# Kernel tuning notes

Measured on AMD Instinct MI355X. Metric: run time of the kernel, lower is better.

Reference implementation:

```python
import jax, jax.numpy as jnp
import numpy as np

N = 1024  # num boxes (labels == predictions count so diff == 0 branch)


def jaccard(box_a, box_b):
    # box_a: [A,4], box_b: [B,4], xyxy format -> IoU matrix [A,B]
    max_xy = jnp.minimum(box_a[:, None, 2:], box_b[None, :, 2:])
    min_xy = jnp.maximum(box_a[:, None, :2], box_b[None, :, :2])
    inter_wh = jnp.clip(max_xy - min_xy, 0.0)
    inter = inter_wh[..., 0] * inter_wh[..., 1]
    area_a = ((box_a[:, 2] - box_a[:, 0]) * (box_a[:, 3] - box_a[:, 1]))[:, None]
    area_b = ((box_b[:, 2] - box_b[:, 0]) * (box_b[:, 3] - box_b[:, 1]))[None, :]
    return inter / (area_a + area_b - inter)


def greedy_match(JM):
    """Replicates the original greedy loop: N steps; each step takes the LAST
    row-major-order maximal entry ('>=' update) among rows/cols not in `seen`,
    swaps label rows r<->c (tracked via perm), and marks column c as seen."""
    n = JM.shape[0]
    MASKED = jnp.float32(-1.0)  # IoU >= 0, so -1 excludes masked entries

    def body(carry, _):
        perm, seen = carry
        M = JM[perm]                                  # rows permuted with labels
        mask = seen[:, None] | seen[None, :]          # one `seen` set for rows & cols
        vals = jnp.where(mask, MASKED, M).reshape(-1)
        # last occurrence of the max (the '>=' in the Python loop keeps the latest)
        i = vals.shape[0] - 1 - jnp.argmax(vals[::-1])
        r, c = i // n, i % n
        pr, pc = perm[r], perm[c]
        perm = perm.at[r].set(pc).at[c].set(pr)
        seen = seen.at[c].set(True)
        return (perm, seen), None

    init = (jnp.arange(n), jnp.zeros(n, dtype=bool))
    (perm, _), _ = jax.lax.scan(body, init, None, length=n)
    return perm


def setup_inputs() -> dict:
    key = jax.random.key(0)
    k1, k2, k3, k4, k5 = jax.random.split(key, 5)
    # valid xyxy boxes: x2 > x1, y2 > y1
    lmin = jax.random.uniform(k1, (N, 2), dtype=jnp.float32)
    lwh = jax.random.uniform(k2, (N, 2), dtype=jnp.float32) * 0.2 + 0.01
    labels = jnp.concatenate([lmin, lmin + lwh], axis=-1)
    pmin = jax.random.uniform(k3, (N, 2), dtype=jnp.float32)
    pwh = jax.random.uniform(k4, (N, 2), dtype=jnp.float32) * 0.2 + 0.01
    predictions = jnp.concatenate([pmin, pmin + pwh], axis=-1)
    scores = jax.random.normal(k5, (N,), dtype=jnp.float32)
    return {"predictions": predictions, "labels": labels, "scores": scores}


def reference(predictions, labels, scores):
    # L == P -> diff == 0, no truncation, scores untouched.
    JM = jaccard(labels, predictions)
    perm = greedy_match(JM)
    labels_matched = labels[perm]
    # F.l1_loss default reduction: mean over all elements.
    # NOTE: the original's `loss.add(F.cross_entropy(...))` is non-in-place and
    # its result is discarded, so the CE term does NOT contribute; diff == 0 so
    # the diff*4 branch is skipped. Faithfully: loss = L1 only.
    loss = jnp.mean(jnp.abs(labels_matched - predictions))
    return loss
```

## Files before the change

kernel.cpp:

```cpp
#include <hip/hip_runtime.h>
#include <stdint.h>

#define NBOX 1024

typedef unsigned long long u64;
typedef unsigned int u32;
typedef unsigned short u16;
typedef unsigned char u8;

__device__ __forceinline__ float iou_pair(const float4 lb, float larea,
                                          const float4 pb, float parea) {
    float ix1 = fmaxf(lb.x, pb.x);
    float iy1 = fmaxf(lb.y, pb.y);
    float ix2 = fminf(lb.z, pb.z);
    float iy2 = fminf(lb.w, pb.w);
    float w = fmaxf(__fsub_rn(ix2, ix1), 0.0f);
    float h = fmaxf(__fsub_rn(iy2, iy1), 0.0f);
    float inter = __fmul_rn(w, h);
    float denom = __fsub_rn(__fadd_rn(larea, parea), inter);
    return inter / denom;
}

__device__ __forceinline__ u64 umax64(u64 a, u64 b) { return a > b ? a : b; }

__device__ __forceinline__ u64 dpp_max64(u64 v) {
    unsigned lo, hi; u64 o;
#define DPP_STEP(CTRL) \
    lo = (unsigned)__builtin_amdgcn_update_dpp(0, (int)(unsigned)(v & 0xffffffffull), CTRL, 0xf, 0xf, true); \
    hi = (unsigned)__builtin_amdgcn_update_dpp(0, (int)(unsigned)(v >> 32),           CTRL, 0xf, 0xf, true); \
    o = (((u64)hi) << 32) | lo; \
    if (o > v) v = o;
    DPP_STEP(0x111) DPP_STEP(0x112) DPP_STEP(0x114)
    DPP_STEP(0x118) DPP_STEP(0x142) DPP_STEP(0x143)
#undef DPP_STEP
    return v;
}

__device__ __forceinline__ u64 readlane64(u64 v, int l) {
    unsigned lo = (unsigned)__builtin_amdgcn_readlane((int)(unsigned)(v & 0xffffffffull), l);
    unsigned hi = (unsigned)__builtin_amdgcn_readlane((int)(unsigned)(v >> 32), l);
    return (((u64)hi) << 32) | lo;
}

__global__ void __launch_bounds__(64) init_rowlist(const float* __restrict__ labels,
                                                   const float* __restrict__ preds,
                                                   u64* __restrict__ rowlist) {
    const int b = blockIdx.x;
    const int lane = threadIdx.x;
    float4 lb = ((const float4*)labels)[b];
    float la = __fmul_rn(__fsub_rn(lb.z, lb.x), __fsub_rn(lb.w, lb.y));
    u32 vb[16];
    #pragma unroll
    for (int j = 0; j < 16; ++j) {
        int c = lane + (j << 6);
        float4 pb = ((const float4*)preds)[c];
        float pa = __fmul_rn(__fsub_rn(pb.z, pb.x), __fsub_rn(pb.w, pb.y));
        vb[j] = __float_as_uint(iou_pair(lb, la, pb, pa));
    }
    u32 used = 0;
    for (int it = 0; it < 8; ++it) {
        u64 best = 0;
        #pragma unroll
        for (int j = 0; j < 16; ++j) {
            if (!((used >> j) & 1u)) {
                u64 p = ((u64)vb[j] << 10) | (u32)(lane + (j << 6));
                best = umax64(best, p);
            }
        }
        best = dpp_max64(best);
        u64 bm = readlane64(best, 63);
        if ((bm >> 10) == 0ull) bm = 0;
        if (lane == 0) rowlist[(b << 3) + it] = bm;
        if (bm && (int)(bm & 63) == lane) used |= 1u << ((bm >> 6) & 15);
    }
}

__global__ void __launch_bounds__(64) init_collist(const float* __restrict__ labels,
                                                   const float* __restrict__ preds,
                                                   u64* __restrict__ collist) {
    const int c = blockIdx.x;
    const int lane = threadIdx.x;
    float4 pc = ((const float4*)preds)[c];
    float pa = __fmul_rn(__fsub_rn(pc.z, pc.x), __fsub_rn(pc.w, pc.y));
    u32 vb[16];
    #pragma unroll
    for (int j = 0; j < 16; ++j) {
        int L = lane + (j << 6);
        float4 lb = ((const float4*)labels)[L];
        float la = __fmul_rn(__fsub_rn(lb.z, lb.x), __fsub_rn(lb.w, lb.y));
        vb[j] = __float_as_uint(iou_pair(lb, la, pc, pa));
    }
    u32 used = 0;
    for (int it = 0; it < 8; ++it) {
        u64 best = 0;
        #pragma unroll
        for (int j = 0; j < 16; ++j) {
            if (!((used >> j) & 1u)) {
                u64 p = ((u64)vb[j] << 10) | (u32)(lane + (j << 6));
                best = umax64(best, p);
            }
        }
        best = dpp_max64(best);
        u64 bm = readlane64(best, 63);
        if ((bm >> 10) == 0ull) bm = 0;
        if (lane == 0) collist[(c << 3) + it] = bm;
        if (bm && (int)(bm & 63) == lane) used |= 1u << ((bm >> 6) & 15);
    }
}

__global__ void __launch_bounds__(1024, 1)
rounds_kernel(const float* __restrict__ preds,
              const float* __restrict__ labels,
              const u64* __restrict__ rowlist,
              const u64* __restrict__ collist,
              float* __restrict__ out) {
    __shared__ float4 pred4s[NBOX];
    __shared__ float4 lab4s[NBOX];
    __shared__ float  parea_s[NBOX];
    __shared__ float  larea_s[NBOX];
    __shared__ u64    rkey[NBOX];
    __shared__ u64    colbest[NBOX];
    __shared__ u16    dest_s[NBOX];
    __shared__ u16    perm_s[NBOX];
    __shared__ u8     seenc[NBOX];
    __shared__ u8     lockedl[NBOX];
    __shared__ u32    seenw[32];
    __shared__ u32    lockedw[32];
    __shared__ int    ncom[2];
    __shared__ float  fpart[16];

    const int t    = (int)threadIdx.x;
    const int lane = t & 63;
    const int wid  = t >> 6;

    {
        float4 p = ((const float4*)preds)[t];
        float4 L = ((const float4*)labels)[t];
        pred4s[t] = p;
        lab4s[t]  = L;
        parea_s[t] = __fmul_rn(__fsub_rn(p.z, p.x), __fsub_rn(p.w, p.y));
        larea_s[t] = __fmul_rn(__fsub_rn(L.z, L.x), __fsub_rn(L.w, L.y));
        perm_s[t] = (u16)t; dest_s[t] = 0;
        seenc[t] = 0; lockedl[t] = 0;
        rkey[t] = rowlist ? rowlist[t << 3] : 0ull;
        colbest[t] = 0ull;
        if (t < 32) { seenw[t] = 0u; lockedw[t] = 0u; }
        if (t < 2) ncom[t] = 0;
    }
    __syncthreads();

    u32 myseen = 0;
    u32 mylocked = 0;
    int rptr = rowlist ? 0 : 8;
    int cptr = collist ? 0 : 8;
    int par = 0;

    auto rebuild_seen = [&]() {
        u32 ms = 0;
        #pragma unroll
        for (int m = 0; m < 4; ++m) {
            u32 w_ = seenw[(lane >> 3) + (m << 3)];
            ms |= ((w_ >> ((lane & 7) << 2)) & 0xFu) << (m << 2);
        }
        myseen = ms;
    };
    auto rebuild_locked = [&]() {
        u32 ml = 0;
        #pragma unroll
        for (int m = 0; m < 4; ++m) {
            u32 w_ = lockedw[(lane >> 3) + (m << 3)];
            ml |= ((w_ >> ((lane & 7) << 2)) & 0xFu) << (m << 2);
        }
        mylocked = ml;
    };

    auto scan_row_exact = [&](int row) -> u64 {
        float4 lbx = lab4s[row];
        float la = larea_s[row];
        u64 best = 0;
        #pragma unroll
        for (int m = 0; m < 4; ++m) {
            #pragma unroll
            for (int k = 0; k < 4; ++k) {
                int cc = 4 * lane + 256 * m + k;
                float v = iou_pair(lbx, la, pred4s[cc], parea_s[cc]);
                u64 p = ((u64)__float_as_uint(v) << 10) | (unsigned)cc;
                if ((myseen >> ((m << 2) | k)) & 1u) p = 0;
                best = umax64(best, p);
            }
        }
        best = dpp_max64(best);
        u64 bm = readlane64(best, 63);
        return (bm >> 10) ? bm : 0ull;
    };

    auto scan_col_exact = [&](int c) -> u64 {
        float4 pc = pred4s[c];
        float  pa = parea_s[c];
        u64 best = 0; u32 v1 = 0, v2 = 0;
        #pragma unroll
        for (int m = 0; m < 4; ++m) {
            #pragma unroll
            for (int k = 0; k < 4; ++k) {
                int L = 4 * lane + 256 * m + k;
                float v = iou_pair(lab4s[L], larea_s[L], pc, pa);
                u32 vbb = __float_as_uint(v);
                if ((mylocked >> ((m << 2) | k)) & 1u) vbb = 0;
                if (vbb >= v1) { v2 = v1; v1 = vbb; } else { v2 = (vbb > v2) ? vbb : v2; }
                best = umax64(best, ((u64)vbb << 10) | (unsigned)L);
            }
        }
        best = dpp_max64(best);
        u64 bm = readlane64(best, 63);
        u32 V = (u32)(bm >> 10);
        if (!V) return 0ull;
        u64 b1 = __ballot(v1 == V);
        u64 b2 = __ballot(v2 == V);
        bool tie = (__popcll(b1) >= 2) || (b2 != 0ull);
        return ((u64)V << 32) | (tie ? (1ull << 16) : 0ull) | (bm & 1023ull);
    };

    auto do_commit = [&](int c, int L) {
        seenc[c] = 1; lockedl[L] = 1; rkey[L] = 0ull;
        dest_s[L] = (u16)c; perm_s[c] = (u16)L;
        atomicOr(&seenw[c >> 5], 1u << (c & 31));
        atomicOr(&lockedw[L >> 5], 1u << (L & 31));
        atomicAdd(&ncom[par], 1);
    };

    if (!rowlist) {
        for (int row = wid; row < NBOX; row += 16) {
            u64 r = scan_row_exact(row);
            if (lane == 0) rkey[row] = r;
        }
        __syncthreads();
    }

    {
        u64 k = rkey[t];
        if (k) atomicMax((unsigned long long*)&colbest[k & 1023ull],
                         ((k >> 10) << 10) | (u64)(unsigned)t);
    }
    __syncthreads();

    for (int round = 0; round < 4096; ++round) {
        par = round & 1;

        u64 sb = colbest[t];
        {
            colbest[t] = 0ull;
            bool needexact = false;
            if (sb) {
                if (cptr >= 8) {
                    needexact = true;
                } else {
                    u32 V = 0, lab1 = 0; bool dead = false;
                    int i = cptr;
                    for (; i < 8; ++i) {
                        u64 e = collist[(t << 3) + i];
                        u32 v = (u32)(e >> 10);
                        if (!v) { dead = true; break; }
                        u32 lb = (u32)(e & 1023ull);
                        if (!lockedl[lb]) { V = v; lab1 = lb; break; }
                    }
                    cptr = i;
                    if (!dead) {
                        if (i >= 8) {
                            needexact = true;
                        } else {
                            bool tie = false;
                            int j = i + 1;
                            for (; j < 8; ++j) {
                                u64 e2 = collist[(t << 3) + j];
                                u32 v2 = (u32)(e2 >> 10);
                                if (v2 != V) break;
                                if (!lockedl[e2 & 1023ull]) { tie = true; break; }
                            }
                            if (!tie && j >= 8) needexact = true;
                            if (!needexact && !tie) {
                                if ((u32)(sb & 1023ull) == lab1) do_commit(t, (int)lab1);
                            }
                        }
                    }
                }
            }
            u64 bal = __ballot(needexact);
            if (bal) {
                rebuild_locked();
                while (bal) {
                    int l = (int)__ffsll(bal) - 1; bal &= bal - 1;
                    int c = (wid << 6) | l;
                    u64 o = scan_col_exact(c);
                    u64 sbl = readlane64(sb, l);
                    if (lane == 0) {
                        u32 Vx = (u32)(o >> 32);
                        if (Vx && !((o >> 16) & 1ull) &&
                            (u32)(o & 1023ull) == (u32)(sbl & 1023ull))
                            do_commit(c, (int)(o & 1023ull));
                    }
                }
            }
        }
        __syncthreads();

        const int cnt = ncom[par];
        if (t == 0) ncom[par ^ 1] = 0;
        if (cnt == 0) break;
        {
            bool needscan = false;
            u64 k = rkey[t];
            if (k && seenc[k & 1023ull]) {
                if (rptr >= 8) {
                    needscan = true;
                } else {
                    int i = rptr; u64 nk = 0;
                    for (; i < 8; ++i) {
                        u64 e = rowlist[(t << 3) + i];
                        if ((e >> 10) == 0ull) break;
                        if (!seenc[e & 1023ull]) { nk = e; break; }
                    }
                    if (i < 8) { rkey[t] = nk; rptr = i; }
                    else { rptr = 8; needscan = true; }
                }
            }
            u64 bal = __ballot(needscan);
            if (bal) {
                rebuild_seen();
                while (bal) {
                    int l = (int)__ffsll(bal) - 1; bal &= bal - 1;
                    int row = (wid << 6) | l;
                    u64 r = scan_row_exact(row);
                    if (lane == 0) rkey[row] = r;
                }
            }
            u64 k2 = rkey[t];
            if (k2) atomicMax((unsigned long long*)&colbest[k2 & 1023ull],
                              ((k2 >> 10) << 10) | (u64)(unsigned)t);
        }
        __syncthreads();
    }

    if (!seenc[t]) {
        int l = t;
        while (lockedl[l]) l = (int)dest_s[l];
        perm_s[t] = (u16)l;
    }
    __syncthreads();

    {
        float4 lb = lab4s[perm_s[t]];
        float4 pb = pred4s[t];
        float sum = fabsf(lb.x - pb.x) + fabsf(lb.y - pb.y) +
                    fabsf(lb.z - pb.z) + fabsf(lb.w - pb.w);
        for (int off = 32; off > 0; off >>= 1) sum += __shfl_xor(sum, off, 64);
        if (lane == 0) fpart[wid] = sum;
        __syncthreads();
        if (t == 0) {
            float s = 0.0f;
            for (int w = 0; w < 16; ++w) s += fpart[w];
            out[0] = s * (1.0f / 4096.0f);
        }
    }
}

extern "C" void kernel_launch(void* const* d_in, const int* in_sizes, int n_in,
                              void* d_out, int out_size, void* d_ws, size_t ws_size,
                              hipStream_t stream) {
    const float* preds  = (const float*)d_in[0];
    const float* labels = (const float*)d_in[1];
    float* out = (float*)d_out;

    const size_t list_b = (size_t)NBOX * 8 * sizeof(u64);
    if (d_ws && ws_size >= 2 * list_b) {
        u64* rl = (u64*)d_ws;
        u64* cl = rl + NBOX * 8;
        init_rowlist<<<NBOX, 64, 0, stream>>>(labels, preds, rl);
        init_collist<<<NBOX, 64, 0, stream>>>(labels, preds, cl);
        rounds_kernel<<<1, 1024, 0, stream>>>(preds, labels, rl, cl, out);
    } else {
        rounds_kernel<<<1, 1024, 0, stream>>>(preds, labels, nullptr, nullptr, out);
    }
}
```

Before: 221.8 us.

## Halve rounds-kernel block to 512 threads, two columns per thread, cache collist in registers

The single-block greedy-matching kernel now runs with 512 threads, each handling two boxes/columns, which cuts the cost of each __syncthreads barrier across the many rounds. Each thread's 8-entry column candidate lists are preloaded into registers once. The per-round column walk becomes a branch-light unrolled check over all 8 entries instead of a pointer-advancing loop over global memory. The risks are higher register pressure, serialization of per-thread work across two items, and possible semantic drift in the tie/exhaustion logic versus the old cursor-based walk.

```diff
diff --git a/kernel.cpp b/kernel.cpp
--- a/kernel.cpp
+++ b/kernel.cpp
@@ -2,6 +2,7 @@
 #include <stdint.h>
 
 #define NBOX 1024
+#define BLK  512
 
 typedef unsigned long long u64;
 typedef unsigned int u32;
@@ -108,7 +109,7 @@
     }
 }
 
-__global__ void __launch_bounds__(1024, 1)
+__global__ void __launch_bounds__(BLK, 1)
 rounds_kernel(const float* __restrict__ preds,
               const float* __restrict__ labels,
               const u64* __restrict__ rowlist,
@@ -127,33 +128,50 @@
     __shared__ u32    seenw[32];
     __shared__ u32    lockedw[32];
     __shared__ int    ncom[2];
-    __shared__ float  fpart[16];
+    __shared__ float  fpart[8];
 
     const int t    = (int)threadIdx.x;
     const int lane = t & 63;
     const int wid  = t >> 6;
 
-    {
-        float4 p = ((const float4*)preds)[t];
-        float4 L = ((const float4*)labels)[t];
-        pred4s[t] = p;
-        lab4s[t]  = L;
-        parea_s[t] = __fmul_rn(__fsub_rn(p.z, p.x), __fsub_rn(p.w, p.y));
-        larea_s[t] = __fmul_rn(__fsub_rn(L.z, L.x), __fsub_rn(L.w, L.y));
-        perm_s[t] = (u16)t; dest_s[t] = 0;
-        seenc[t] = 0; lockedl[t] = 0;
-        rkey[t] = rowlist ? rowlist[t << 3] : 0ull;
-        colbest[t] = 0ull;
-        if (t < 32) { seenw[t] = 0u; lockedw[t] = 0u; }
-        if (t < 2) ncom[t] = 0;
-    }
+    #pragma unroll
+    for (int s = 0; s < 2; ++s) {
+        int i = t + (s << 9);
+        float4 p = ((const float4*)preds)[i];
+        float4 L = ((const float4*)labels)[i];
+        pred4s[i] = p;
+        lab4s[i]  = L;
+        parea_s[i] = __fmul_rn(__fsub_rn(p.z, p.x), __fsub_rn(p.w, p.y));
+        larea_s[i] = __fmul_rn(__fsub_rn(L.z, L.x), __fsub_rn(L.w, L.y));
+        perm_s[i] = (u16)i; dest_s[i] = 0;
+        seenc[i] = 0; lockedl[i] = 0;
+        rkey[i] = rowlist ? rowlist[i << 3] : 0ull;
+        colbest[i] = 0ull;
+    }
+    if (t < 32) { seenw[t] = 0u; lockedw[t] = 0u; }
+    if (t < 2) ncom[t] = 0;
     __syncthreads();
+
+    u32 cvA[8], clA[8], cvB[8], clB[8];
+    if (collist) {
+        #pragma unroll
+        for (int k = 0; k < 8; ++k) {
+            u64 e = collist[(t << 3) + k];
+            cvA[k] = (u32)(e >> 10); clA[k] = (u32)(e & 1023ull);
+            e = collist[((t + 512) << 3) + k];
+            cvB[k] = (u32)(e >> 10); clB[k] = (u32)(e & 1023ull);
+        }
+    } else {
+        #pragma unroll
+        for (int k = 0; k < 8; ++k) { cvA[k] = clA[k] = cvB[k] = clB[k] = 0; }
+    }
 
     u32 myseen = 0;
     u32 mylocked = 0;
-    int rptr = rowlist ? 0 : 8;
-    int cptr = collist ? 0 : 8;
+    int rptr0 = rowlist ? 0 : 8;
+    int rptr1 = rowlist ? 0 : 8;
     int par = 0;
+    const bool havelists = (collist != nullptr);
 
     auto rebuild_seen = [&]() {
         u32 ms = 0;
@@ -228,78 +246,86 @@
         atomicAdd(&ncom[par], 1);
     };
 
+#define COLWALK(CV, CL, cidx, sbv, needx) do { \
+        if (!havelists) { needx = true; } else { \
+            bool lk_[8]; \
+            _Pragma("unroll") \
+            for (int k = 0; k < 8; ++k) lk_[k] = lockedl[CL[k]]; \
+            u32 fm_ = 0; \
+            _Pragma("unroll") \
+            for (int k = 0; k < 8; ++k) if (CV[k] && !lk_[k]) fm_ |= 1u << k; \
+            if (!fm_) { if (CV[7]) needx = true;  } \
+            else { \
+                u32 V_ = 0, lab_ = 0; \
+                _Pragma("unroll") \
+                for (int k = 7; k >= 0; --k) \
+                    if ((fm_ >> k) & 1u) { V_ = CV[k]; lab_ = CL[k]; } \
+                u32 eq_ = 0; \
+                _Pragma("unroll") \
+                for (int k = 0; k < 8; ++k) if (CV[k] == V_) eq_ |= 1u << k; \
+                bool tie_ = __popc(fm_ & eq_) >= 2; \
+                if (!tie_) { \
+                    if (CV[7] == V_) needx = true;               \
+                    else if ((u32)((sbv) & 1023ull) == lab_) do_commit((cidx), (int)lab_); \
+                }  \
+            } \
+        } } while (0)
+
     if (!rowlist) {
-        for (int row = wid; row < NBOX; row += 16) {
+        for (int row = wid; row < NBOX; row += 8) {
             u64 r = scan_row_exact(row);
             if (lane == 0) rkey[row] = r;
         }
         __syncthreads();
     }
 
-    {
-        u64 k = rkey[t];
+    #pragma unroll
+    for (int s = 0; s < 2; ++s) {
+        u64 k = rkey[t + (s << 9)];
         if (k) atomicMax((unsigned long long*)&colbest[k & 1023ull],
-                         ((k >> 10) << 10) | (u64)(unsigned)t);
+                         ((k >> 10) << 10) | (u64)(unsigned)(t + (s << 9)));
     }
     __syncthreads();
 
     for (int round = 0; round < 4096; ++round) {
         par = round & 1;
 
-        u64 sb = colbest[t];
         {
-            colbest[t] = 0ull;
-            bool needexact = false;
-            if (sb) {
-                if (cptr >= 8) {
-                    needexact = true;
-                } else {
-                    u32 V = 0, lab1 = 0; bool dead = false;
-                    int i = cptr;
-                    for (; i < 8; ++i) {
-                        u64 e = collist[(t << 3) + i];
-                        u32 v = (u32)(e >> 10);
-                        if (!v) { dead = true; break; }
-                        u32 lb = (u32)(e & 1023ull);
-                        if (!lockedl[lb]) { V = v; lab1 = lb; break; }
-                    }
-                    cptr = i;
-                    if (!dead) {
-                        if (i >= 8) {
-                            needexact = true;
-                        } else {
-                            bool tie = false;
-                            int j = i + 1;
-                            for (; j < 8; ++j) {
-                                u64 e2 = collist[(t << 3) + j];
-                                u32 v2 = (u32)(e2 >> 10);
-                                if (v2 != V) break;
-                                if (!lockedl[e2 & 1023ull]) { tie = true; break; }
-                            }
-                            if (!tie && j >= 8) needexact = true;
-                            if (!needexact && !tie) {
-                                if ((u32)(sb & 1023ull) == lab1) do_commit(t, (int)lab1);
-                            }
-                        }
-                    }
-                }
-            }
-            u64 bal = __ballot(needexact);
+            u64 sb0 = colbest[t];       colbest[t] = 0ull;
+            u64 sb1 = colbest[t + 512]; colbest[t + 512] = 0ull;
+            bool ne0 = false, ne1 = false;
+            if (sb0) COLWALK(cvA, clA, t, sb0, ne0);
+            if (sb1) COLWALK(cvB, clB, t + 512, sb1, ne1);
+            u64 bal = __ballot(ne0);
             if (bal) {
                 rebuild_locked();
                 while (bal) {
                     int l = (int)__ffsll(bal) - 1; bal &= bal - 1;
                     int c = (wid << 6) | l;
                     u64 o = scan_col_exact(c);
-                    u64 sbl = readlane64(sb, l);
+                    u64 sbl = readlane64(sb0, l);
                     if (lane == 0) {
-                        u32 Vx = (u32)(o >> 32);
-                        if (Vx && !((o >> 16) & 1ull) &&
+                        if ((o >> 32) && !((o >> 16) & 1ull) &&
                             (u32)(o & 1023ull) == (u32)(sbl & 1023ull))
                             do_commit(c, (int)(o & 1023ull));
                     }
                 }
             }
+            bal = __ballot(ne1);
+            if (bal) {
+                rebuild_locked();
+                while (bal) {
+                    int l = (int)__ffsll(bal) - 1; bal &= bal - 1;
+                    int c = 512 + ((wid << 6) | l);
+                    u64 o = scan_col_exact(c);
+                    u64 sbl = readlane64(sb1, l);
+                    if (lane == 0) {
+                        if ((o >> 32) && !((o >> 16) & 1ull) &&
+                            (u32)(o & 1023ull) == (u32)(sbl & 1023ull))
+                            do_commit(c, (int)(o & 1023ull));
+                    }
+                }
+            }
         }
         __syncthreads();
 
@@ -307,23 +333,30 @@
         if (t == 0) ncom[par ^ 1] = 0;
         if (cnt == 0) break;
         {
-            bool needscan = false;
-            u64 k = rkey[t];
-            if (k && seenc[k & 1023ull]) {
-                if (rptr >= 8) {
-                    needscan = true;
-                } else {
-                    int i = rptr; u64 nk = 0;
-                    for (; i < 8; ++i) {
-                        u64 e = rowlist[(t << 3) + i];
-                        if ((e >> 10) == 0ull) break;
-                        if (!seenc[e & 1023ull]) { nk = e; break; }
+            bool ns0 = false, ns1 = false;
+            #pragma unroll
+            for (int s = 0; s < 2; ++s) {
+                int row = t + (s << 9);
+                int rp = s ? rptr1 : rptr0;
+                bool needscan = false;
+                u64 k = rkey[row];
+                if (k && seenc[k & 1023ull]) {
+                    if (rp >= 8) {
+                        needscan = true;
+                    } else {
+                        int i = rp; u64 nk = 0;
+                        for (; i < 8; ++i) {
+                            u64 e = rowlist[(row << 3) + i];
+                            if ((e >> 10) == 0ull) break;
+                            if (!seenc[e & 1023ull]) { nk = e; break; }
+                        }
+                        if (i < 8) { rkey[row] = nk; rp = i; }
+                        else { rp = 8; needscan = true; }
                     }
-                    if (i < 8) { rkey[t] = nk; rptr = i; }
-                    else { rptr = 8; needscan = true; }
                 }
-            }
-            u64 bal = __ballot(needscan);
+                if (s) { rptr1 = rp; ns1 = needscan; } else { rptr0 = rp; ns0 = needscan; }
+            }
+            u64 bal = __ballot(ns0);
             if (bal) {
                 rebuild_seen();
                 while (bal) {
@@ -333,31 +366,54 @@
                     if (lane == 0) rkey[row] = r;
                 }
             }
-            u64 k2 = rkey[t];
-            if (k2) atomicMax((unsigned long long*)&colbest[k2 & 1023ull],
-                              ((k2 >> 10) << 10) | (u64)(unsigned)t);
+            bal = __ballot(ns1);
+            if (bal) {
+                rebuild_seen();
+                while (bal) {
+                    int l = (int)__ffsll(bal) - 1; bal &= bal - 1;
+                    int row = 512 + ((wid << 6) | l);
+                    u64 r = scan_row_exact(row);
+                    if (lane == 0) rkey[row] = r;
+                }
+            }
+            #pragma unroll
+            for (int s = 0; s < 2; ++s) {
+                int row = t + (s << 9);
+                u64 k2 = rkey[row];
+                if (k2) atomicMax((unsigned long long*)&colbest[k2 & 1023ull],
+                                  ((k2 >> 10) << 10) | (u64)(unsigned)row);
+            }
         }
         __syncthreads();
     }
 
-    if (!seenc[t]) {
-        int l = t;
-        while (lockedl[l]) l = (int)dest_s[l];
-        perm_s[t] = (u16)l;
+    #pragma unroll
+    for (int s = 0; s < 2; ++s) {
+        int i = t + (s << 9);
+        if (!seenc[i]) {
+            int l = i;
+            while (lockedl[l]) l = (int)dest_s[l];
+            perm_s[i] = (u16)l;
+        }
     }
     __syncthreads();
 
     {
-        float4 lb = lab4s[perm_s[t]];
-        float4 pb = pred4s[t];
-        float sum = fabsf(lb.x - pb.x) + fabsf(lb.y - pb.y) +
-                    fabsf(lb.z - pb.z) + fabsf(lb.w - pb.w);
+        float sum = 0.0f;
+        #pragma unroll
+        for (int s = 0; s < 2; ++s) {
+            int i = t + (s << 9);
+            float4 lb = lab4s[perm_s[i]];
+            float4 pb = pred4s[i];
+            sum += fabsf(lb.x - pb.x) + fabsf(lb.y - pb.y) +
+                   fabsf(lb.z - pb.z) + fabsf(lb.w - pb.w);
+        }
         for (int off = 32; off > 0; off >>= 1) sum += __shfl_xor(sum, off, 64);
         if (lane == 0) fpart[wid] = sum;
         __syncthreads();
         if (t == 0) {
             float s = 0.0f;
-            for (int w = 0; w < 16; ++w) s += fpart[w];
+            for (int w = 0; w < 8; ++w) s += fpart[w];
             out[0] = s * (1.0f / 4096.0f);
         }
     }
@@ -376,8 +432,8 @@
         u64* cl = rl + NBOX * 8;
         init_rowlist<<<NBOX, 64, 0, stream>>>(labels, preds, rl);
         init_collist<<<NBOX, 64, 0, stream>>>(labels, preds, cl);
-        rounds_kernel<<<1, 1024, 0, stream>>>(preds, labels, rl, cl, out);
+        rounds_kernel<<<1, BLK, 0, stream>>>(preds, labels, rl, cl, out);
     } else {
-        rounds_kernel<<<1, 1024, 0, stream>>>(preds, labels, nullptr, nullptr, out);
-    }
-}
+        rounds_kernel<<<1, BLK, 0, stream>>>(preds, labels, nullptr, nullptr, out);
+    }
+}
```

After: 223.5 us. No clear change (+0.8%).
